# Optimization experiments

Measured on AMD Instinct MI355X. Metric: run time of the kernel, lower is better.

Reference implementation:

```python
import jax, jax.numpy as jnp
import numpy as np

N, D_IN = 65536, 512
H1, H2, D_SH = 1024, 1024, 512   # shared net: num_nodes_shared = [1024, 1024, 512]
HI = 512                          # indiv hidden width, num_nodes_indiv = [512, 512]


def setup_inputs() -> dict:
    key = jax.random.key(0)
    ks = jax.random.split(key, 16)
    s = 0.02
    inp = {
        "input": jax.random.normal(ks[0], (N, D_IN), jnp.float32),
        "treatment": jax.random.randint(ks[1], (N,), 0, 2, jnp.int32),
        # shared net (hidden ReLU layers + linear output, all with bias)
        "W0": jax.random.normal(ks[2], (D_IN, H1), jnp.float32) * s,
        "b0": jnp.zeros((H1,), jnp.float32),
        "W1": jax.random.normal(ks[3], (H1, H2), jnp.float32) * s,
        "b1": jnp.zeros((H2,), jnp.float32),
        "W2": jax.random.normal(ks[4], (H2, D_SH), jnp.float32) * s,
        "b2": jnp.zeros((D_SH,), jnp.float32),
        # risk net 0 (output layer has no bias)
        "A0": jax.random.normal(ks[5], (D_SH, HI), jnp.float32) * s,
        "a0": jnp.zeros((HI,), jnp.float32),
        "A1": jax.random.normal(ks[6], (HI, HI), jnp.float32) * s,
        "a1": jnp.zeros((HI,), jnp.float32),
        "A2": jax.random.normal(ks[7], (HI, 1), jnp.float32) * s,
        # risk net 1
        "C0": jax.random.normal(ks[8], (D_SH, HI), jnp.float32) * s,
        "c0": jnp.zeros((HI,), jnp.float32),
        "C1": jax.random.normal(ks[9], (HI, HI), jnp.float32) * s,
        "c1": jnp.zeros((HI,), jnp.float32),
        "C2": jax.random.normal(ks[10], (HI, 1), jnp.float32) * s,
    }
    return inp


def _risk_net(h, U0, u0, U1, u1, U2):
    h = jax.nn.relu(h @ U0 + u0)
    h = jax.nn.relu(h @ U1 + u1)
    return h @ U2  # [N, 1], no output bias


def reference(input, treatment, W0, b0, W1, b1, W2, b2,
              A0, a0, A1, a1, A2, C0, c0, C1, c1, C2):
    # shared MLP
    h = jax.nn.relu(input @ W0 + b0)
    h = jax.nn.relu(h @ W1 + b1)
    out = h @ W2 + b2                     # [N, D_SH]
    # Binary expert routing. The torch code gathers samples per treatment,
    # runs each group through its own MLP and scatters results back; the
    # math is equivalent to applying both experts and selecting per sample.
    y0 = _risk_net(out, A0, a0, A1, a1, A2)[:, 0]  # [N]
    y1 = _risk_net(out, C0, c0, C1, c1, C2)[:, 0]  # [N]
    y = jnp.where(treatment == 0, y0, y1)          # [N]
    return (y, out)
```

## Files before the change

kernel.cpp:

```cpp
#include <hip/hip_runtime.h>
#include <hip/hip_bf16.h>
#include <stdint.h>

typedef short short8 __attribute__((ext_vector_type(8)));
typedef float f32x4 __attribute__((ext_vector_type(4)));

#define NSAMP 65536
#define AS1 __attribute__((address_space(1)))
#define AS3 __attribute__((address_space(3)))

__device__ __forceinline__ unsigned f2bf(float f) {
    union { float f; unsigned u; } v; v.f = f;
    unsigned u = v.u;
    u += 0x7fffu + ((u >> 16) & 1u);
    return u >> 16;
}


__global__ void k_convert_bf16(const float* __restrict__ in, unsigned short* __restrict__ out, int n8) {
    int i = blockIdx.x * blockDim.x + threadIdx.x;
    if (i >= n8) return;
    const float4* p = (const float4*)in + (size_t)i * 2;
    float4 a = p[0], b = p[1];
    short8 o;
    o[0] = (short)f2bf(a.x); o[1] = (short)f2bf(a.y);
    o[2] = (short)f2bf(a.z); o[3] = (short)f2bf(a.w);
    o[4] = (short)f2bf(b.x); o[5] = (short)f2bf(b.y);
    o[6] = (short)f2bf(b.z); o[7] = (short)f2bf(b.w);
    ((short8*)out)[i] = o;
}

struct PrepArgs {
    const float *W0, *W1, *W2, *A0, *C0, *A1, *C1, *a0v, *c0v;
    unsigned short *W0T, *W1T, *W2T, *RT0, *A1T, *C1T;
    float *bcat, *yout;
};
__global__ void k_prep(PrepArgs p) {
    int i = blockIdx.x * blockDim.x + threadIdx.x;
    if (i < 524288)  { int k = i >> 10, n = i & 1023; p.W0T[n * 512 + k] = f2bf(p.W0[i]); return; }
    i -= 524288;
    if (i < 1048576) { int k = i >> 10, n = i & 1023; p.W1T[n * 1024 + k] = f2bf(p.W1[i]); return; }
    i -= 1048576;
    if (i < 524288)  { int k = i >> 9, n = i & 511; p.W2T[n * 1024 + k] = f2bf(p.W2[i]); return; }
    i -= 524288;
    if (i < 262144)  { int k = i >> 9, n = i & 511; p.RT0[n * 512 + k] = f2bf(p.A0[i]); return; }
    i -= 262144;
    if (i < 262144)  { int k = i >> 9, n = i & 511; p.RT0[(512 + n) * 512 + k] = f2bf(p.C0[i]); return; }
    i -= 262144;
    if (i < 262144)  { int k = i >> 9, n = i & 511; p.A1T[n * 512 + k] = f2bf(p.A1[i]); return; }
    i -= 262144;
    if (i < 262144)  { int k = i >> 9, n = i & 511; p.C1T[n * 512 + k] = f2bf(p.C1[i]); return; }
    i -= 262144;
    if (i < 512)     { p.bcat[i] = p.a0v[i]; return; }
    i -= 512;
    if (i < 512)     { p.bcat[512 + i] = p.c0v[i]; return; }
    i -= 512;
    if (i < 65536)   { p.yout[i] = 0.f; return; }
}

template<int MODE>
__global__ __launch_bounds__(512, 2)
void k_gemm256(const unsigned short* __restrict__ A, int lda,
               const unsigned short* __restrict__ BT, const unsigned short* __restrict__ BT2,
               const float* __restrict__ bias, const float* __restrict__ bias2,
               unsigned short* __restrict__ Cbf, float* __restrict__ Cf32,
               const float* __restrict__ w2, const float* __restrict__ w2b,
               const int* __restrict__ TRt, float* __restrict__ ydot,
               int Ncols, int K, int TPB)
{
    __shared__ __align__(16) char lds[131072];

    const int tid  = threadIdx.x;
    const int lane = tid & 63;
    const int wid  = tid >> 6;
    const int wr   = wid >> 2;
    const int wcn  = wid & 3;

    const int bid = (int)((blockIdx.x & 7) * 32 + (blockIdx.x >> 3));
    const int cls = bid % TPB;
    const int w   = bid / TPB;
    const int MSTEP = 256 / TPB;

    int n0e, cOff = 0, expert = 0;
    const unsigned short* Bsel = BT;
    if (MODE == 2) {
        expert = cls >> 1;
        n0e = (cls & 1) << 8;
        cOff = expert << 9;
        if (expert) Bsel = BT2;
    } else {
        n0e = cls << 8;
    }

    const int srow = tid >> 2;
    const int scs  = (tid & 3) ^ ((srow >> 1) & 3);
    const int ldst = wid * 1024;

    const unsigned short* gB0 = Bsel + (size_t)(n0e + srow) * K + scs * 8;
    const unsigned short* gB1 = gB0 + (size_t)128 * K;
    const size_t dA = (size_t)MSTEP * 256 * lda;
    const unsigned short* cA0 = A + (size_t)((w << 8) + srow) * lda + cOff + scs * 8;
    const unsigned short* cA1 = cA0 + (size_t)128 * lda;

#define STAGE_BLK(dbuf, blkoff, g0, g1, koff)                                            \
    do {                                                                                 \
        __builtin_amdgcn_global_load_lds((const AS1 void*)((g0) + (koff)),               \
                                         (AS3 void*)((dbuf) + (blkoff) + ldst), 16, 0, 0); \
        __builtin_amdgcn_global_load_lds((const AS1 void*)((g1) + (koff)),               \
                                         (AS3 void*)((dbuf) + (blkoff) + 8192 + ldst), 16, 0, 0); \
    } while (0)

    int aOff[8], bOff[4];
#pragma unroll
    for (int i = 0; i < 8; ++i) {
        int r = wr * 128 + i * 16 + (lane & 15);
        aOff[i] = r * 64 + ((((lane >> 4) ^ ((r >> 1) & 3))) << 4);
    }
#pragma unroll
    for (int j = 0; j < 4; ++j) {
        int r = wcn * 64 + j * 16 + (lane & 15);
        bOff[j] = r * 64 + ((((lane >> 4) ^ ((r >> 1) & 3))) << 4);
    }

    f32x4 acc[8][4];
#pragma unroll
    for (int i = 0; i < 8; ++i)
#pragma unroll
        for (int j = 0; j < 4; ++j) acc[i][j] = (f32x4)0.f;

    const int KT  = K >> 6;
    const int TOT = TPB * KT;

    STAGE_BLK(lds, 0,     cA0, cA1, 0);
    STAGE_BLK(lds, 32768, gB0, gB1, 0);
    STAGE_BLK(lds, 16384, cA0, cA1, 32);
    STAGE_BLK(lds, 49152, gB0, gB1, 32);
    asm volatile("s_waitcnt vmcnt(4)" ::: "memory");
    __builtin_amdgcn_s_barrier();
    __builtin_amdgcn_sched_barrier(0);

    short8 pa[4], pb[4];
#pragma unroll
    for (int i = 0; i < 4; ++i) pa[i] = *(const short8*)(lds + aOff[i]);
#pragma unroll
    for (int j = 0; j < 4; ++j) pb[j] = *(const short8*)(lds + 32768 + bOff[j]);

    int g = 0;
    for (int tau = 0; tau < TPB; ++tau) {
        const unsigned short* nA0 = cA0 + dA;
        const unsigned short* nA1 = cA1 + dA;

        for (int t = 0; t < KT; ++t, ++g) {
            const char* sbuf = lds + (g & 1) * 65536;
            char* dbuf = lds + ((g + 1) & 1) * 65536;
            const bool inTile = (t + 1 < KT);
            const bool st = (g + 1 < TOT);
            const unsigned short* sA0 = inTile ? cA0 : nA0;
            const unsigned short* sA1 = inTile ? cA1 : nA1;
            const int koff = inTile ? ((t + 1) << 6) : 0;
            short8 xa[4];

            if (st) {
                STAGE_BLK(dbuf, 0,     sA0, sA1, koff);
                STAGE_BLK(dbuf, 32768, gB0, gB1, koff);
            }
#pragma unroll
            for (int i = 0; i < 4; ++i) xa[i] = *(const short8*)(sbuf + aOff[4 + i]);
            __builtin_amdgcn_s_setprio(1);
#pragma unroll
            for (int i = 0; i < 4; ++i)
#pragma unroll
                for (int j = 0; j < 4; ++j)
                    acc[i][j] = __builtin_amdgcn_mfma_f32_16x16x32_bf16(pb[j], pa[i], acc[i][j], 0, 0, 0);
            __builtin_amdgcn_s_setprio(0);

            __builtin_amdgcn_s_setprio(1);
#pragma unroll
            for (int i = 0; i < 4; ++i)
#pragma unroll
                for (int j = 0; j < 4; ++j)
                    acc[4 + i][j] = __builtin_amdgcn_mfma_f32_16x16x32_bf16(pb[j], xa[i], acc[4 + i][j], 0, 0, 0);
            __builtin_amdgcn_s_setprio(0);
            if (st) { asm volatile("s_waitcnt vmcnt(4)" ::: "memory"); }
            else    { asm volatile("s_waitcnt vmcnt(0)" ::: "memory"); }
            __builtin_amdgcn_sched_barrier(0);
            __builtin_amdgcn_s_barrier();
            __builtin_amdgcn_sched_barrier(0);

#pragma unroll
            for (int i = 0; i < 4; ++i) pa[i] = *(const short8*)(sbuf + 16384 + aOff[i]);
#pragma unroll
            for (int j = 0; j < 4; ++j) pb[j] = *(const short8*)(sbuf + 49152 + bOff[j]);
            if (st) {
                STAGE_BLK(dbuf, 16384, sA0, sA1, koff + 32);
                STAGE_BLK(dbuf, 49152, gB0, gB1, koff + 32);
            }
            __builtin_amdgcn_s_setprio(1);
#pragma unroll
            for (int i = 0; i < 4; ++i)
#pragma unroll
                for (int j = 0; j < 4; ++j)
                    acc[i][j] = __builtin_amdgcn_mfma_f32_16x16x32_bf16(pb[j], pa[i], acc[i][j], 0, 0, 0);
            __builtin_amdgcn_s_setprio(0);

#pragma unroll
            for (int i = 0; i < 4; ++i) xa[i] = *(const short8*)(sbuf + 16384 + aOff[4 + i]);
            __builtin_amdgcn_s_setprio(1);
#pragma unroll
            for (int i = 0; i < 4; ++i)
#pragma unroll
                for (int j = 0; j < 4; ++j)
                    acc[4 + i][j] = __builtin_amdgcn_mfma_f32_16x16x32_bf16(pb[j], xa[i], acc[4 + i][j], 0, 0, 0);
            __builtin_amdgcn_s_setprio(0);
            if (st) {
                asm volatile("s_waitcnt vmcnt(4)" ::: "memory");
                __builtin_amdgcn_sched_barrier(0);
                __builtin_amdgcn_s_barrier();
                __builtin_amdgcn_sched_barrier(0);
#pragma unroll
                for (int i = 0; i < 4; ++i) pa[i] = *(const short8*)(dbuf + aOff[i]);
#pragma unroll
                for (int j = 0; j < 4; ++j) pb[j] = *(const short8*)(dbuf + 32768 + bOff[j]);
            }
        }

        const int m0 = (w + MSTEP * tau) << 8;
        if (MODE == 2) {
            const float* be = expert ? bias2 : bias;
            const float* we = expert ? w2b : w2;
            const int nb = n0e + wcn * 64 + ((lane >> 4) << 2);
            f32x4 bv[4], wv[4];
#pragma unroll
            for (int j = 0; j < 4; ++j) {
                bv[j] = *(const f32x4*)(be + nb + j * 16);
                wv[j] = *(const f32x4*)(we + nb + j * 16);
            }
#pragma unroll
            for (int i = 0; i < 8; ++i) {
                float p = 0.f;
#pragma unroll
                for (int j = 0; j < 4; ++j)
#pragma unroll
                    for (int r = 0; r < 4; ++r)
                        p += fmaxf(acc[i][j][r] + bv[j][r], 0.f) * wv[j][r];
                p += __shfl_xor(p, 16);
                p += __shfl_xor(p, 32);
                const int m = m0 + wr * 128 + i * 16 + (lane & 15);
                if (lane < 16 && TRt[m] == expert) atomicAdd(&ydot[m], p);
            }
        } else {
            const int nb = n0e + wcn * 64 + ((lane >> 4) << 2);
            f32x4 bv[4];
#pragma unroll
            for (int j = 0; j < 4; ++j) bv[j] = *(const f32x4*)(bias + nb + j * 16);
#pragma unroll
            for (int i = 0; i < 8; ++i) {
                const int m = m0 + wr * 128 + i * 16 + (lane & 15);
                unsigned short* pbc = Cbf + (size_t)m * Ncols + nb;
#pragma unroll
                for (int j = 0; j < 4; ++j) {
                    f32x4 v = acc[i][j] + bv[j];
                    if (MODE == 0) {
#pragma unroll
                        for (int r = 0; r < 4; ++r) v[r] = fmaxf(v[r], 0.f);
                    }
                    if (MODE == 1) *(f32x4*)(Cf32 + (size_t)m * Ncols + nb + j * 16) = v;
                    unsigned long long pk =
                        (unsigned long long)(f2bf(v[0]) | (f2bf(v[1]) << 16)) |
                        ((unsigned long long)(f2bf(v[2]) | (f2bf(v[3]) << 16)) << 32);
                    *(unsigned long long*)(pbc + j * 16) = pk;
                }
            }
        }

#pragma unroll
        for (int i = 0; i < 8; ++i)
#pragma unroll
            for (int j = 0; j < 4; ++j) acc[i][j] = (f32x4)0.f;
        cA0 = nA0; cA1 = nA1;
    }
#undef STAGE_BLK
}


extern "C" void kernel_launch(void* const* d_in, const int* in_sizes, int n_in,
                              void* d_out, int out_size, void* d_ws, size_t ws_size,
                              hipStream_t stream) {
    const float* X  = (const float*)d_in[0];
    const int*  TR  = (const int*)d_in[1];
    const float* W0 = (const float*)d_in[2];  const float* b0 = (const float*)d_in[3];
    const float* W1 = (const float*)d_in[4];  const float* b1 = (const float*)d_in[5];
    const float* W2 = (const float*)d_in[6];  const float* b2 = (const float*)d_in[7];
    const float* A0 = (const float*)d_in[8];  const float* a0 = (const float*)d_in[9];
    const float* A1 = (const float*)d_in[10]; const float* a1 = (const float*)d_in[11];
    const float* A2 = (const float*)d_in[12];
    const float* C0 = (const float*)d_in[13]; const float* c0 = (const float*)d_in[14];
    const float* C1 = (const float*)d_in[15]; const float* c1 = (const float*)d_in[16];
    const float* C2 = (const float*)d_in[17];

    float* y_out   = (float*)d_out;
    float* out_out = (float*)d_out + NSAMP;

    char* ws = (char*)d_ws;
    size_t off = 0;
    auto alloc = [&](size_t bytes) -> char* {
        char* p = ws + off;
        off += (bytes + 255) & ~(size_t)255;
        return p;
    };
    unsigned short* Xb  = (unsigned short*)alloc((size_t)NSAMP * 512 * 2);
    unsigned short* H1b = (unsigned short*)alloc((size_t)NSAMP * 1024 * 2);
    unsigned short* H2b = (unsigned short*)alloc((size_t)NSAMP * 1024 * 2);
    unsigned short* OUTb = H1b;
    unsigned short* R01  = H2b;
    unsigned short* W0T = (unsigned short*)alloc(512 * 1024 * 2);
    unsigned short* W1T = (unsigned short*)alloc(1024 * 1024 * 2);
    unsigned short* W2T = (unsigned short*)alloc(1024 * 512 * 2);
    unsigned short* RT0 = (unsigned short*)alloc(1024 * 512 * 2);
    unsigned short* A1T = (unsigned short*)alloc(512 * 512 * 2);
    unsigned short* C1T = (unsigned short*)alloc(512 * 512 * 2);
    float* bcat = (float*)alloc(1024 * 4);

    k_convert_bf16<<<(NSAMP * 512 / 8 + 255) / 256, 256, 0, stream>>>(X, Xb, NSAMP * 512 / 8);
    PrepArgs pa;
    pa.W0 = W0; pa.W1 = W1; pa.W2 = W2; pa.A0 = A0; pa.C0 = C0; pa.A1 = A1; pa.C1 = C1;
    pa.a0v = a0; pa.c0v = c0;
    pa.W0T = W0T; pa.W1T = W1T; pa.W2T = W2T; pa.RT0 = RT0; pa.A1T = A1T; pa.C1T = C1T;
    pa.bcat = bcat; pa.yout = y_out;
    k_prep<<<(3212288 + 255) / 256, 256, 0, stream>>>(pa);

    k_gemm256<0><<<256, 512, 0, stream>>>(Xb, 512, W0T, nullptr, b0, nullptr,
                                          H1b, nullptr, nullptr, nullptr, nullptr, nullptr,
                                          1024, 512, 4);
    k_gemm256<0><<<256, 512, 0, stream>>>(H1b, 1024, W1T, nullptr, b1, nullptr,
                                          H2b, nullptr, nullptr, nullptr, nullptr, nullptr,
                                          1024, 1024, 4);
    k_gemm256<1><<<256, 512, 0, stream>>>(H2b, 1024, W2T, nullptr, b2, nullptr,
                                          OUTb, out_out, nullptr, nullptr, nullptr, nullptr,
                                          512, 1024, 2);

    k_gemm256<0><<<256, 512, 0, stream>>>(OUTb, 512, RT0, nullptr, bcat, nullptr,
                                          R01, nullptr, nullptr, nullptr, nullptr, nullptr,
                                          1024, 512, 4);

    k_gemm256<2><<<256, 512, 0, stream>>>(R01, 1024, A1T, C1T, a1, c1,
                                          nullptr, nullptr, A2, C2, TR, y_out,
                                          512, 512, 4);
}
```

Baseline: 573.0 us.

## Switch GEMM to 32x32x16 MFMA tiles and fold input conversion into prep

The GEMM inner loop now uses 32x32x16 bf16 MFMA instructions with 16-wide accumulators instead of 16x16x32. The LDS offsets and the epilogue mappings for bias, ReLU, stores and the expert dot-product are rewritten to match the 32x32 output layout. The larger MFMA halves the instruction count per tile and uses fewer LDS fragment reads per FLOP. Separately, the fp32-to-bf16 input conversion is merged into the prep kernel, which removes one launch. The new epilogue reads bias and weight vectors per fragment and issues the y atomics from 32 lanes instead of 16.

```diff
diff --git a/kernel.cpp b/kernel.cpp
--- a/kernel.cpp
+++ b/kernel.cpp
@@ -3,7 +3,8 @@
 #include <stdint.h>
 
 typedef short short8 __attribute__((ext_vector_type(8)));
-typedef float f32x4 __attribute__((ext_vector_type(4)));
+typedef float f32x4  __attribute__((ext_vector_type(4)));
+typedef float f32x16 __attribute__((ext_vector_type(16)));
 
 #define NSAMP 65536
 #define AS1 __attribute__((address_space(1)))
@@ -16,27 +17,25 @@
     return u >> 16;
 }
 
-
-__global__ void k_convert_bf16(const float* __restrict__ in, unsigned short* __restrict__ out, int n8) {
-    int i = blockIdx.x * blockDim.x + threadIdx.x;
-    if (i >= n8) return;
-    const float4* p = (const float4*)in + (size_t)i * 2;
-    float4 a = p[0], b = p[1];
-    short8 o;
-    o[0] = (short)f2bf(a.x); o[1] = (short)f2bf(a.y);
-    o[2] = (short)f2bf(a.z); o[3] = (short)f2bf(a.w);
-    o[4] = (short)f2bf(b.x); o[5] = (short)f2bf(b.y);
-    o[6] = (short)f2bf(b.z); o[7] = (short)f2bf(b.w);
-    ((short8*)out)[i] = o;
-}
-
 struct PrepArgs {
-    const float *W0, *W1, *W2, *A0, *C0, *A1, *C1, *a0v, *c0v;
-    unsigned short *W0T, *W1T, *W2T, *RT0, *A1T, *C1T;
+    const float *X, *W0, *W1, *W2, *A0, *C0, *A1, *C1, *a0v, *c0v;
+    unsigned short *Xb, *W0T, *W1T, *W2T, *RT0, *A1T, *C1T;
     float *bcat, *yout;
 };
 __global__ void k_prep(PrepArgs p) {
     int i = blockIdx.x * blockDim.x + threadIdx.x;
+    if (i < 4194304) {
+        const float4* q = (const float4*)p.X + (size_t)i * 2;
+        float4 a = q[0], b = q[1];
+        short8 o;
+        o[0] = (short)f2bf(a.x); o[1] = (short)f2bf(a.y);
+        o[2] = (short)f2bf(a.z); o[3] = (short)f2bf(a.w);
+        o[4] = (short)f2bf(b.x); o[5] = (short)f2bf(b.y);
+        o[6] = (short)f2bf(b.z); o[7] = (short)f2bf(b.w);
+        ((short8*)p.Xb)[i] = o;
+        return;
+    }
+    i -= 4194304;
     if (i < 524288)  { int k = i >> 10, n = i & 1023; p.W0T[n * 512 + k] = f2bf(p.W0[i]); return; }
     i -= 524288;
     if (i < 1048576) { int k = i >> 10, n = i & 1023; p.W1T[n * 1024 + k] = f2bf(p.W1[i]); return; }
@@ -110,23 +109,29 @@
                                          (AS3 void*)((dbuf) + (blkoff) + 8192 + ldst), 16, 0, 0); \
     } while (0)
 
-    int aOff[8], bOff[4];
-#pragma unroll
-    for (int i = 0; i < 8; ++i) {
-        int r = wr * 128 + i * 16 + (lane & 15);
-        aOff[i] = r * 64 + ((((lane >> 4) ^ ((r >> 1) & 3))) << 4);
-    }
-#pragma unroll
-    for (int j = 0; j < 4; ++j) {
-        int r = wcn * 64 + j * 16 + (lane & 15);
-        bOff[j] = r * 64 + ((((lane >> 4) ^ ((r >> 1) & 3))) << 4);
-    }
-
-    f32x4 acc[8][4];
-#pragma unroll
-    for (int i = 0; i < 8; ++i)
-#pragma unroll
-        for (int j = 0; j < 4; ++j) acc[i][j] = (f32x4)0.f;
+    const int oct = lane >> 5;
+    const int rl  = lane & 31;
+    int aOff[4][2], bOff[4];
+#pragma unroll
+    for (int mi = 0; mi < 4; ++mi) {
+        int r = wr * 128 + mi * 32 + rl;
+#pragma unroll
+        for (int s = 0; s < 2; ++s)
+            aOff[mi][s] = r * 64 + (((2 * s + oct) ^ ((r >> 1) & 3)) << 4);
+    }
+#pragma unroll
+    for (int nj = 0; nj < 2; ++nj) {
+        int r = wcn * 64 + nj * 32 + rl;
+#pragma unroll
+        for (int s = 0; s < 2; ++s)
+            bOff[nj * 2 + s] = r * 64 + (((2 * s + oct) ^ ((r >> 1) & 3)) << 4);
+    }
+
+    f32x16 acc[4][2];
+#pragma unroll
+    for (int mi = 0; mi < 4; ++mi)
+#pragma unroll
+        for (int nj = 0; nj < 2; ++nj) acc[mi][nj] = (f32x16)0.f;
 
     const int KT  = K >> 6;
     const int TOT = TPB * KT;
@@ -141,9 +146,9 @@
 
     short8 pa[4], pb[4];
 #pragma unroll
-    for (int i = 0; i < 4; ++i) pa[i] = *(const short8*)(lds + aOff[i]);
-#pragma unroll
-    for (int j = 0; j < 4; ++j) pb[j] = *(const short8*)(lds + 32768 + bOff[j]);
+    for (int mi = 0; mi < 4; ++mi) pa[mi] = *(const short8*)(lds + aOff[mi][0]);
+#pragma unroll
+    for (int b = 0; b < 4; ++b)    pb[b]  = *(const short8*)(lds + 32768 + bOff[b]);
 
     int g = 0;
     for (int tau = 0; tau < TPB; ++tau) {
@@ -165,21 +170,21 @@
                 STAGE_BLK(dbuf, 32768, gB0, gB1, koff);
             }
 #pragma unroll
-            for (int i = 0; i < 4; ++i) xa[i] = *(const short8*)(sbuf + aOff[4 + i]);
+            for (int mi = 0; mi < 4; ++mi) xa[mi] = *(const short8*)(sbuf + aOff[mi][1]);
             __builtin_amdgcn_s_setprio(1);
 #pragma unroll
-            for (int i = 0; i < 4; ++i)
-#pragma unroll
-                for (int j = 0; j < 4; ++j)
-                    acc[i][j] = __builtin_amdgcn_mfma_f32_16x16x32_bf16(pb[j], pa[i], acc[i][j], 0, 0, 0);
+            for (int mi = 0; mi < 4; ++mi)
+#pragma unroll
+                for (int nj = 0; nj < 2; ++nj)
+                    acc[mi][nj] = __builtin_amdgcn_mfma_f32_32x32x16_bf16(pb[nj * 2], pa[mi], acc[mi][nj], 0, 0, 0);
             __builtin_amdgcn_s_setprio(0);
 
             __builtin_amdgcn_s_setprio(1);
 #pragma unroll
-            for (int i = 0; i < 4; ++i)
-#pragma unroll
-                for (int j = 0; j < 4; ++j)
-                    acc[4 + i][j] = __builtin_amdgcn_mfma_f32_16x16x32_bf16(pb[j], xa[i], acc[4 + i][j], 0, 0, 0);
+            for (int mi = 0; mi < 4; ++mi)
+#pragma unroll
+                for (int nj = 0; nj < 2; ++nj)
+                    acc[mi][nj] = __builtin_amdgcn_mfma_f32_32x32x16_bf16(pb[nj * 2 + 1], xa[mi], acc[mi][nj], 0, 0, 0);
             __builtin_amdgcn_s_setprio(0);
             if (st) { asm volatile("s_waitcnt vmcnt(4)" ::: "memory"); }
             else    { asm volatile("s_waitcnt vmcnt(0)" ::: "memory"); }
@@ -188,29 +193,29 @@
             __builtin_amdgcn_sched_barrier(0);
 
 #pragma unroll
-            for (int i = 0; i < 4; ++i) pa[i] = *(const short8*)(sbuf + 16384 + aOff[i]);
-#pragma unroll
-            for (int j = 0; j < 4; ++j) pb[j] = *(const short8*)(sbuf + 49152 + bOff[j]);
+            for (int mi = 0; mi < 4; ++mi) pa[mi] = *(const short8*)(sbuf + 16384 + aOff[mi][0]);
+#pragma unroll
+            for (int b = 0; b < 4; ++b)    pb[b]  = *(const short8*)(sbuf + 49152 + bOff[b]);
             if (st) {
                 STAGE_BLK(dbuf, 16384, sA0, sA1, koff + 32);
                 STAGE_BLK(dbuf, 49152, gB0, gB1, koff + 32);
             }
             __builtin_amdgcn_s_setprio(1);
 #pragma unroll
-            for (int i = 0; i < 4; ++i)
-#pragma unroll
-                for (int j = 0; j < 4; ++j)
-                    acc[i][j] = __builtin_amdgcn_mfma_f32_16x16x32_bf16(pb[j], pa[i], acc[i][j], 0, 0, 0);
+            for (int mi = 0; mi < 4; ++mi)
+#pragma unroll
+                for (int nj = 0; nj < 2; ++nj)
+                    acc[mi][nj] = __builtin_amdgcn_mfma_f32_32x32x16_bf16(pb[nj * 2], pa[mi], acc[mi][nj], 0, 0, 0);
             __builtin_amdgcn_s_setprio(0);
 
 #pragma unroll
-            for (int i = 0; i < 4; ++i) xa[i] = *(const short8*)(sbuf + 16384 + aOff[4 + i]);
+            for (int mi = 0; mi < 4; ++mi) xa[mi] = *(const short8*)(sbuf + 16384 + aOff[mi][1]);
             __builtin_amdgcn_s_setprio(1);
 #pragma unroll
-            for (int i = 0; i < 4; ++i)
-#pragma unroll
-                for (int j = 0; j < 4; ++j)
-                    acc[4 + i][j] = __builtin_amdgcn_mfma_f32_16x16x32_bf16(pb[j], xa[i], acc[4 + i][j], 0, 0, 0);
+            for (int mi = 0; mi < 4; ++mi)
+#pragma unroll
+                for (int nj = 0; nj < 2; ++nj)
+                    acc[mi][nj] = __builtin_amdgcn_mfma_f32_32x32x16_bf16(pb[nj * 2 + 1], xa[mi], acc[mi][nj], 0, 0, 0);
             __builtin_amdgcn_s_setprio(0);
             if (st) {
                 asm volatile("s_waitcnt vmcnt(4)" ::: "memory");
@@ -218,9 +223,9 @@
                 __builtin_amdgcn_s_barrier();
                 __builtin_amdgcn_sched_barrier(0);
 #pragma unroll
-                for (int i = 0; i < 4; ++i) pa[i] = *(const short8*)(dbuf + aOff[i]);
-#pragma unroll
-                for (int j = 0; j < 4; ++j) pb[j] = *(const short8*)(dbuf + 32768 + bOff[j]);
+                for (int mi = 0; mi < 4; ++mi) pa[mi] = *(const short8*)(dbuf + aOff[mi][0]);
+#pragma unroll
+                for (int b = 0; b < 4; ++b)    pb[b]  = *(const short8*)(dbuf + 32768 + bOff[b]);
             }
         }
 
@@ -228,55 +233,55 @@
         if (MODE == 2) {
             const float* be = expert ? bias2 : bias;
             const float* we = expert ? w2b : w2;
-            const int nb = n0e + wcn * 64 + ((lane >> 4) << 2);
-            f32x4 bv[4], wv[4];
-#pragma unroll
-            for (int j = 0; j < 4; ++j) {
-                bv[j] = *(const f32x4*)(be + nb + j * 16);
-                wv[j] = *(const f32x4*)(we + nb + j * 16);
-            }
-#pragma unroll
-            for (int i = 0; i < 8; ++i) {
+#pragma unroll
+            for (int mi = 0; mi < 4; ++mi) {
                 float p = 0.f;
 #pragma unroll
-                for (int j = 0; j < 4; ++j)
-#pragma unroll
-                    for (int r = 0; r < 4; ++r)
-                        p += fmaxf(acc[i][j][r] + bv[j][r], 0.f) * wv[j][r];
-                p += __shfl_xor(p, 16);
+                for (int nj = 0; nj < 2; ++nj) {
+                    const int nb = n0e + wcn * 64 + nj * 32 + 4 * oct;
+#pragma unroll
+                    for (int q = 0; q < 4; ++q) {
+                        f32x4 bv = *(const f32x4*)(be + nb + 8 * q);
+                        f32x4 wv = *(const f32x4*)(we + nb + 8 * q);
+#pragma unroll
+                        for (int r = 0; r < 4; ++r)
+                            p += fmaxf(acc[mi][nj][4 * q + r] + bv[r], 0.f) * wv[r];
+                    }
+                }
                 p += __shfl_xor(p, 32);
-                const int m = m0 + wr * 128 + i * 16 + (lane & 15);
-                if (lane < 16 && TRt[m] == expert) atomicAdd(&ydot[m], p);
+                const int m = m0 + wr * 128 + mi * 32 + rl;
+                if (lane < 32 && TRt[m] == expert) atomicAdd(&ydot[m], p);
             }
         } else {
-            const int nb = n0e + wcn * 64 + ((lane >> 4) << 2);
-            f32x4 bv[4];
-#pragma unroll
-            for (int j = 0; j < 4; ++j) bv[j] = *(const f32x4*)(bias + nb + j * 16);
-#pragma unroll
-            for (int i = 0; i < 8; ++i) {
-                const int m = m0 + wr * 128 + i * 16 + (lane & 15);
-                unsigned short* pbc = Cbf + (size_t)m * Ncols + nb;
-#pragma unroll
-                for (int j = 0; j < 4; ++j) {
-                    f32x4 v = acc[i][j] + bv[j];
-                    if (MODE == 0) {
-#pragma unroll
-                        for (int r = 0; r < 4; ++r) v[r] = fmaxf(v[r], 0.f);
+#pragma unroll
+            for (int mi = 0; mi < 4; ++mi) {
+                const int m = m0 + wr * 128 + mi * 32 + rl;
+#pragma unroll
+                for (int nj = 0; nj < 2; ++nj) {
+                    const int nb = n0e + wcn * 64 + nj * 32 + 4 * oct;
+#pragma unroll
+                    for (int q = 0; q < 4; ++q) {
+                        f32x4 v;
+                        f32x4 bv = *(const f32x4*)(bias + nb + 8 * q);
+#pragma unroll
+                        for (int r = 0; r < 4; ++r) {
+                            v[r] = acc[mi][nj][4 * q + r] + bv[r];
+                            if (MODE == 0) v[r] = fmaxf(v[r], 0.f);
+                        }
+                        if (MODE == 1) *(f32x4*)(Cf32 + (size_t)m * Ncols + nb + 8 * q) = v;
+                        unsigned long long pk =
+                            (unsigned long long)(f2bf(v[0]) | (f2bf(v[1]) << 16)) |
+                            ((unsigned long long)(f2bf(v[2]) | (f2bf(v[3]) << 16)) << 32);
+                        *(unsigned long long*)(Cbf + (size_t)m * Ncols + nb + 8 * q) = pk;
                     }
-                    if (MODE == 1) *(f32x4*)(Cf32 + (size_t)m * Ncols + nb + j * 16) = v;
-                    unsigned long long pk =
-                        (unsigned long long)(f2bf(v[0]) | (f2bf(v[1]) << 16)) |
-                        ((unsigned long long)(f2bf(v[2]) | (f2bf(v[3]) << 16)) << 32);
-                    *(unsigned long long*)(pbc + j * 16) = pk;
                 }
             }
         }
 
 #pragma unroll
-        for (int i = 0; i < 8; ++i)
-#pragma unroll
-            for (int j = 0; j < 4; ++j) acc[i][j] = (f32x4)0.f;
+        for (int mi = 0; mi < 4; ++mi)
+#pragma unroll
+            for (int nj = 0; nj < 2; ++nj) acc[mi][nj] = (f32x16)0.f;
         cA0 = nA0; cA1 = nA1;
     }
 #undef STAGE_BLK
@@ -321,13 +326,13 @@
     unsigned short* C1T = (unsigned short*)alloc(512 * 512 * 2);
     float* bcat = (float*)alloc(1024 * 4);
 
-    k_convert_bf16<<<(NSAMP * 512 / 8 + 255) / 256, 256, 0, stream>>>(X, Xb, NSAMP * 512 / 8);
     PrepArgs pa;
+    pa.X = X;
     pa.W0 = W0; pa.W1 = W1; pa.W2 = W2; pa.A0 = A0; pa.C0 = C0; pa.A1 = A1; pa.C1 = C1;
     pa.a0v = a0; pa.c0v = c0;
-    pa.W0T = W0T; pa.W1T = W1T; pa.W2T = W2T; pa.RT0 = RT0; pa.A1T = A1T; pa.C1T = C1T;
+    pa.Xb = Xb; pa.W0T = W0T; pa.W1T = W1T; pa.W2T = W2T; pa.RT0 = RT0; pa.A1T = A1T; pa.C1T = C1T;
     pa.bcat = bcat; pa.yout = y_out;
-    k_prep<<<(3212288 + 255) / 256, 256, 0, stream>>>(pa);
+    k_prep<<<(7406592 + 255) / 256, 256, 0, stream>>>(pa);
 
     k_gemm256<0><<<256, 512, 0, stream>>>(Xb, 512, W0T, nullptr, b0, nullptr,
                                           H1b, nullptr, nullptr, nullptr, nullptr, nullptr,
```

Measured after the change: 634.5 us. +10.7%, slower.

## Fuse fp32-to-bf16 input conversion into first GEMM's A-tile staging

Applied to the files above, without the earlier changes.

Removes the separate conversion kernel and its bf16 copy of the input. The first GEMM now loads fp32 input rows into registers, converts them to bf16, and writes them into the LDS A-tile. B tiles still use the async global-to-LDS path, and wait counts are adjusted for the extra loads. This avoids a full write and reread of the bf16 input. In exchange it adds register pressure, VALU conversion work and synchronous LDS writes inside the first GEMM's pipelined loop.

```diff
diff --git a/kernel.cpp b/kernel.cpp
--- a/kernel.cpp
+++ b/kernel.cpp
@@ -16,18 +16,13 @@
     return u >> 16;
 }
 
-
-__global__ void k_convert_bf16(const float* __restrict__ in, unsigned short* __restrict__ out, int n8) {
-    int i = blockIdx.x * blockDim.x + threadIdx.x;
-    if (i >= n8) return;
-    const float4* p = (const float4*)in + (size_t)i * 2;
-    float4 a = p[0], b = p[1];
+__device__ __forceinline__ void wr8(char* d, f32x4 a, f32x4 b) {
     short8 o;
-    o[0] = (short)f2bf(a.x); o[1] = (short)f2bf(a.y);
-    o[2] = (short)f2bf(a.z); o[3] = (short)f2bf(a.w);
-    o[4] = (short)f2bf(b.x); o[5] = (short)f2bf(b.y);
-    o[6] = (short)f2bf(b.z); o[7] = (short)f2bf(b.w);
-    ((short8*)out)[i] = o;
+    o[0] = (short)f2bf(a[0]); o[1] = (short)f2bf(a[1]);
+    o[2] = (short)f2bf(a[2]); o[3] = (short)f2bf(a[3]);
+    o[4] = (short)f2bf(b[0]); o[5] = (short)f2bf(b[1]);
+    o[6] = (short)f2bf(b[2]); o[7] = (short)f2bf(b[3]);
+    *(short8*)d = o;
 }
 
 struct PrepArgs {
@@ -60,7 +55,7 @@
 
 template<int MODE>
 __global__ __launch_bounds__(512, 2)
-void k_gemm256(const unsigned short* __restrict__ A, int lda,
+void k_gemm256(const void* __restrict__ Av, int lda,
                const unsigned short* __restrict__ BT, const unsigned short* __restrict__ BT2,
                const float* __restrict__ bias, const float* __restrict__ bias2,
                unsigned short* __restrict__ Cbf, float* __restrict__ Cf32,
@@ -98,9 +93,13 @@
 
     const unsigned short* gB0 = Bsel + (size_t)(n0e + srow) * K + scs * 8;
     const unsigned short* gB1 = gB0 + (size_t)128 * K;
+
+    const unsigned short* Ab = (const unsigned short*)Av;
+    const float*          Af = (const float*)Av;
     const size_t dA = (size_t)MSTEP * 256 * lda;
-    const unsigned short* cA0 = A + (size_t)((w << 8) + srow) * lda + cOff + scs * 8;
+    const unsigned short* cA0 = Ab + (size_t)((w << 8) + srow) * lda + cOff + scs * 8;
     const unsigned short* cA1 = cA0 + (size_t)128 * lda;
+    const float* cF = Af + (size_t)((w << 8) + srow) * lda + scs * 8;
 
 #define STAGE_BLK(dbuf, blkoff, g0, g1, koff)                                            \
     do {                                                                                 \
@@ -131,11 +130,29 @@
     const int KT  = K >> 6;
     const int TOT = TPB * KT;
 
-    STAGE_BLK(lds, 0,     cA0, cA1, 0);
-    STAGE_BLK(lds, 32768, gB0, gB1, 0);
-    STAGE_BLK(lds, 16384, cA0, cA1, 32);
-    STAGE_BLK(lds, 49152, gB0, gB1, 32);
-    asm volatile("s_waitcnt vmcnt(4)" ::: "memory");
+    f32x4 xr0, xr1, xr2, xr3;
+    f32x4 yr0, yr1, yr2, yr3;
+
+    if constexpr (MODE == 3) {
+        xr0 = *(const f32x4*)(cF);                xr1 = *(const f32x4*)(cF + 4);
+        xr2 = *(const f32x4*)(cF + 128 * lda);    xr3 = *(const f32x4*)(cF + 128 * lda + 4);
+        STAGE_BLK(lds, 32768, gB0, gB1, 0);
+        __builtin_amdgcn_sched_barrier(0);
+        yr0 = *(const f32x4*)(cF + 32);             yr1 = *(const f32x4*)(cF + 36);
+        yr2 = *(const f32x4*)(cF + 128 * lda + 32); yr3 = *(const f32x4*)(cF + 128 * lda + 36);
+        STAGE_BLK(lds, 49152, gB0, gB1, 32);
+        __builtin_amdgcn_sched_barrier(0);
+        wr8(lds + tid * 16, xr0, xr1);
+        wr8(lds + 8192 + tid * 16, xr2, xr3);
+        asm volatile("s_waitcnt vmcnt(6)" ::: "memory");
+        asm volatile("s_waitcnt lgkmcnt(0)" ::: "memory");
+    } else {
+        STAGE_BLK(lds, 0,     cA0, cA1, 0);
+        STAGE_BLK(lds, 32768, gB0, gB1, 0);
+        STAGE_BLK(lds, 16384, cA0, cA1, 32);
+        STAGE_BLK(lds, 49152, gB0, gB1, 32);
+        asm volatile("s_waitcnt vmcnt(4)" ::: "memory");
+    }
     __builtin_amdgcn_s_barrier();
     __builtin_amdgcn_sched_barrier(0);
 
@@ -149,20 +166,33 @@
     for (int tau = 0; tau < TPB; ++tau) {
         const unsigned short* nA0 = cA0 + dA;
         const unsigned short* nA1 = cA1 + dA;
+        const float* nF = cF + dA;
 
         for (int t = 0; t < KT; ++t, ++g) {
-            const char* sbuf = lds + (g & 1) * 65536;
+            char* sbuf = lds + (g & 1) * 65536;
             char* dbuf = lds + ((g + 1) & 1) * 65536;
             const bool inTile = (t + 1 < KT);
             const bool st = (g + 1 < TOT);
             const unsigned short* sA0 = inTile ? cA0 : nA0;
             const unsigned short* sA1 = inTile ? cA1 : nA1;
+            const float* sF = inTile ? cF : nF;
             const int koff = inTile ? ((t + 1) << 6) : 0;
             short8 xa[4];
 
-            if (st) {
-                STAGE_BLK(dbuf, 0,     sA0, sA1, koff);
-                STAGE_BLK(dbuf, 32768, gB0, gB1, koff);
+            if constexpr (MODE == 3) {
+                wr8(sbuf + 16384 + tid * 16, yr0, yr1);
+                wr8(sbuf + 16384 + 8192 + tid * 16, yr2, yr3);
+                if (st) {
+                    xr0 = *(const f32x4*)(sF + koff);               xr1 = *(const f32x4*)(sF + koff + 4);
+                    xr2 = *(const f32x4*)(sF + 128 * lda + koff);   xr3 = *(const f32x4*)(sF + 128 * lda + koff + 4);
+                    STAGE_BLK(dbuf, 32768, gB0, gB1, koff);
+                    __builtin_amdgcn_sched_barrier(0);
+                }
+            } else {
+                if (st) {
+                    STAGE_BLK(dbuf, 0,     sA0, sA1, koff);
+                    STAGE_BLK(dbuf, 32768, gB0, gB1, koff);
+                }
             }
 #pragma unroll
             for (int i = 0; i < 4; ++i) xa[i] = *(const short8*)(sbuf + aOff[4 + i]);
@@ -181,8 +211,13 @@
                 for (int j = 0; j < 4; ++j)
                     acc[4 + i][j] = __builtin_amdgcn_mfma_f32_16x16x32_bf16(pb[j], xa[i], acc[4 + i][j], 0, 0, 0);
             __builtin_amdgcn_s_setprio(0);
-            if (st) { asm volatile("s_waitcnt vmcnt(4)" ::: "memory"); }
-            else    { asm volatile("s_waitcnt vmcnt(0)" ::: "memory"); }
+            if (st) {
+                if constexpr (MODE == 3) { asm volatile("s_waitcnt vmcnt(6)" ::: "memory"); }
+                else                     { asm volatile("s_waitcnt vmcnt(4)" ::: "memory"); }
+            } else {
+                asm volatile("s_waitcnt vmcnt(0)" ::: "memory");
+            }
+            if constexpr (MODE == 3) { asm volatile("s_waitcnt lgkmcnt(0)" ::: "memory"); }
             __builtin_amdgcn_sched_barrier(0);
             __builtin_amdgcn_s_barrier();
             __builtin_amdgcn_sched_barrier(0);
@@ -191,9 +226,18 @@
             for (int i = 0; i < 4; ++i) pa[i] = *(const short8*)(sbuf + 16384 + aOff[i]);
 #pragma unroll
             for (int j = 0; j < 4; ++j) pb[j] = *(const short8*)(sbuf + 49152 + bOff[j]);
-            if (st) {
-                STAGE_BLK(dbuf, 16384, sA0, sA1, koff + 32);
-                STAGE_BLK(dbuf, 49152, gB0, gB1, koff + 32);
+            if constexpr (MODE == 3) {
+                if (st) {
+                    yr0 = *(const f32x4*)(sF + koff + 32);             yr1 = *(const f32x4*)(sF + koff + 36);
+                    yr2 = *(const f32x4*)(sF + 128 * lda + koff + 32); yr3 = *(const f32x4*)(sF + 128 * lda + koff + 36);
+                    STAGE_BLK(dbuf, 49152, gB0, gB1, koff + 32);
+                    __builtin_amdgcn_sched_barrier(0);
+                }
+            } else {
+                if (st) {
+                    STAGE_BLK(dbuf, 16384, sA0, sA1, koff + 32);
+                    STAGE_BLK(dbuf, 49152, gB0, gB1, koff + 32);
+                }
             }
             __builtin_amdgcn_s_setprio(1);
 #pragma unroll
@@ -213,7 +257,14 @@
                     acc[4 + i][j] = __builtin_amdgcn_mfma_f32_16x16x32_bf16(pb[j], xa[i], acc[4 + i][j], 0, 0, 0);
             __builtin_amdgcn_s_setprio(0);
             if (st) {
-                asm volatile("s_waitcnt vmcnt(4)" ::: "memory");
+                if constexpr (MODE == 3) {
+                    asm volatile("s_waitcnt vmcnt(6)" ::: "memory");
+                    wr8(dbuf + tid * 16, xr0, xr1);
+                    wr8(dbuf + 8192 + tid * 16, xr2, xr3);
+                    asm volatile("s_waitcnt lgkmcnt(0)" ::: "memory");
+                } else {
+                    asm volatile("s_waitcnt vmcnt(4)" ::: "memory");
+                }
                 __builtin_amdgcn_sched_barrier(0);
                 __builtin_amdgcn_s_barrier();
                 __builtin_amdgcn_sched_barrier(0);
@@ -260,7 +311,7 @@
 #pragma unroll
                 for (int j = 0; j < 4; ++j) {
                     f32x4 v = acc[i][j] + bv[j];
-                    if (MODE == 0) {
+                    if (MODE != 1) {
 #pragma unroll
                         for (int r = 0; r < 4; ++r) v[r] = fmaxf(v[r], 0.f);
                     }
@@ -277,7 +328,7 @@
         for (int i = 0; i < 8; ++i)
 #pragma unroll
             for (int j = 0; j < 4; ++j) acc[i][j] = (f32x4)0.f;
-        cA0 = nA0; cA1 = nA1;
+        cA0 = nA0; cA1 = nA1; cF = nF;
     }
 #undef STAGE_BLK
 }
@@ -308,7 +359,6 @@
         off += (bytes + 255) & ~(size_t)255;
         return p;
     };
-    unsigned short* Xb  = (unsigned short*)alloc((size_t)NSAMP * 512 * 2);
     unsigned short* H1b = (unsigned short*)alloc((size_t)NSAMP * 1024 * 2);
     unsigned short* H2b = (unsigned short*)alloc((size_t)NSAMP * 1024 * 2);
     unsigned short* OUTb = H1b;
@@ -321,7 +371,6 @@
     unsigned short* C1T = (unsigned short*)alloc(512 * 512 * 2);
     float* bcat = (float*)alloc(1024 * 4);
 
-    k_convert_bf16<<<(NSAMP * 512 / 8 + 255) / 256, 256, 0, stream>>>(X, Xb, NSAMP * 512 / 8);
     PrepArgs pa;
     pa.W0 = W0; pa.W1 = W1; pa.W2 = W2; pa.A0 = A0; pa.C0 = C0; pa.A1 = A1; pa.C1 = C1;
     pa.a0v = a0; pa.c0v = c0;
@@ -329,21 +378,21 @@
     pa.bcat = bcat; pa.yout = y_out;
     k_prep<<<(3212288 + 255) / 256, 256, 0, stream>>>(pa);
 
-    k_gemm256<0><<<256, 512, 0, stream>>>(Xb, 512, W0T, nullptr, b0, nullptr,
+    k_gemm256<3><<<256, 512, 0, stream>>>((const void*)X, 512, W0T, nullptr, b0, nullptr,
                                           H1b, nullptr, nullptr, nullptr, nullptr, nullptr,
                                           1024, 512, 4);
-    k_gemm256<0><<<256, 512, 0, stream>>>(H1b, 1024, W1T, nullptr, b1, nullptr,
+    k_gemm256<0><<<256, 512, 0, stream>>>((const void*)H1b, 1024, W1T, nullptr, b1, nullptr,
                                           H2b, nullptr, nullptr, nullptr, nullptr, nullptr,
                                           1024, 1024, 4);
-    k_gemm256<1><<<256, 512, 0, stream>>>(H2b, 1024, W2T, nullptr, b2, nullptr,
+    k_gemm256<1><<<256, 512, 0, stream>>>((const void*)H2b, 1024, W2T, nullptr, b2, nullptr,
                                           OUTb, out_out, nullptr, nullptr, nullptr, nullptr,
                                           512, 1024, 2);
 
-    k_gemm256<0><<<256, 512, 0, stream>>>(OUTb, 512, RT0, nullptr, bcat, nullptr,
+    k_gemm256<0><<<256, 512, 0, stream>>>((const void*)OUTb, 512, RT0, nullptr, bcat, nullptr,
                                           R01, nullptr, nullptr, nullptr, nullptr, nullptr,
                                           1024, 512, 4);
 
-    k_gemm256<2><<<256, 512, 0, stream>>>(R01, 1024, A1T, C1T, a1, c1,
+    k_gemm256<2><<<256, 512, 0, stream>>>((const void*)R01, 1024, A1T, C1T, a1, c1,
                                           nullptr, nullptr, A2, C2, TR, y_out,
                                           512, 512, 4);
 }
```

Result: no change. 565.2 us (-1.4%).
